# Kernel optimization log

Measured on AMD Instinct MI355X. Metric: run time of the kernel, lower is better.

Reference implementation:

```python
import jax, jax.numpy as jnp
import numpy as np

H = 8
DH = 64
SCALE = DH ** -0.5

def setup_inputs() -> dict:
    key = jax.random.key(0)
    ks = jax.random.split(key, 32)
    B, NQ, N1, N2, N3 = 4, 1024, 1024, 1024, 2048
    QD, C1, C2, C3 = 512, 512, 768, 256
    INNER, VD = H * DH, 512
    s = 0.02
    inp = {
        'x':        jax.random.normal(ks[0], (B, NQ, QD), jnp.float32),
        'context':  jax.random.normal(ks[1], (B, N1, C1), jnp.float32),
        'context2': jax.random.normal(ks[2], (B, N2, C2), jnp.float32),
        'context3': jax.random.normal(ks[3], (B, N3, C3), jnp.float32),
        'mask1': jax.random.randint(ks[4], (B, NQ, N1), 0, 2) > 0,
        'mask2': jax.random.randint(ks[5], (B, NQ, N2), 0, 2) > 0,
        'mask3': jax.random.randint(ks[6], (B, NQ, N3), 0, 2) > 0,
        'Wq':  jax.random.normal(ks[7],  (QD, INNER), jnp.float32) * s,
        'bq':  jnp.zeros((INNER,), jnp.float32),
        'Wk1': jax.random.normal(ks[8],  (C1, INNER), jnp.float32) * s,
        'bk1': jnp.zeros((INNER,), jnp.float32),
        'Wv1': jax.random.normal(ks[9],  (C1, VD), jnp.float32) * s,
        'bv1': jnp.zeros((VD,), jnp.float32),
        'Wk2': jax.random.normal(ks[10], (C2, INNER), jnp.float32) * s,
        'bk2': jnp.zeros((INNER,), jnp.float32),
        'Wv2': jax.random.normal(ks[11], (C2, VD), jnp.float32) * s,
        'bv2': jnp.zeros((VD,), jnp.float32),
        'Wk3': jax.random.normal(ks[12], (C3, INNER), jnp.float32) * s,
        'bk3': jnp.zeros((INNER,), jnp.float32),
        'Wv3': jax.random.normal(ks[13], (C3, VD), jnp.float32) * s,
        'bv3': jnp.zeros((VD,), jnp.float32),
        'Wo':  jax.random.normal(ks[14], (VD, VD), jnp.float32) * s,
        'bo':  jnp.zeros((VD,), jnp.float32),
    }
    return inp

def _split_heads(t):
    # [b, n, h*d] -> [b, h, n, d]
    b, n, hd = t.shape
    return t.reshape(b, n, H, hd // H).transpose(0, 2, 1, 3)

def reference(x, context, context2, context3, mask1, mask2, mask3,
              Wq, bq, Wk1, bk1, Wv1, bv1, Wk2, bk2, Wv2, bv2,
              Wk3, bk3, Wv3, bv3, Wo, bo):
    q = x @ Wq + bq
    k = jnp.concatenate([context @ Wk1 + bk1, context2 @ Wk2 + bk2, context3 @ Wk3 + bk3], axis=1)
    v = jnp.concatenate([context @ Wv1 + bv1, context2 @ Wv2 + bv2, context3 @ Wv3 + bv3], axis=1)
    qh, kh, vh = _split_heads(q), _split_heads(k), _split_heads(v)
    sim = jnp.einsum('bhid,bhjd->bhij', qh, kh) * SCALE  # [b,h,nq,nk]
    mask = jnp.concatenate([mask1, mask2, mask3], axis=2)  # [b,nq,nk]
    neg = -jnp.finfo(sim.dtype).max
    sim = jnp.where(mask[:, None, :, :], sim, neg)
    attn = jax.nn.softmax(sim, axis=-1)
    out = jnp.einsum('bhij,bhjd->bhid', attn, vh)  # [b,h,nq,dv]
    b, h, n, d = out.shape
    out = out.transpose(0, 2, 1, 3).reshape(b, n, h * d)
    return out @ Wo + bo
```

## Files before the change

### kernel.cpp

```cpp
#include <hip/hip_runtime.h>

typedef _Float16 f16;
typedef _Float16 f16x8 __attribute__((ext_vector_type(8)));
typedef _Float16 f16x4 __attribute__((ext_vector_type(4)));
typedef float f32x4 __attribute__((ext_vector_type(4)));
typedef unsigned long long u64;

#define MFMA16(a, b, c) __builtin_amdgcn_mfma_f32_16x16x32_f16((a), (b), (c), 0, 0, 0)

constexpr float QSCALE = 0.18033688011112042f;

struct CDesc { const float* src; f16* dst; unsigned n4, off4; };

__global__ __launch_bounds__(256) void convert_kernel(CDesc a, CDesc b, CDesc c, CDesc d) {
  unsigned t = blockIdx.x * 256u + threadIdx.x;
  CDesc s;
  if (t >= d.off4) s = d;
  else if (t >= c.off4) s = c;
  else if (t >= b.off4) s = b;
  else s = a;
  unsigned i = t - s.off4;
  if (i >= s.n4) return;
  float4 v = ((const float4*)s.src)[i];
  f16x4 o;
  o[0] = (f16)v.x; o[1] = (f16)v.y; o[2] = (f16)v.z; o[3] = (f16)v.w;
  ((f16x4*)s.dst)[i] = o;
}

struct TDesc { const float* src; f16* dst; int K, blk_off; };
struct TArgs { TDesc t[8]; };

__global__ __launch_bounds__(256) void transpose_kernel(TArgs args) {
  int bid = blockIdx.x;
  int di = 0;
#pragma unroll
  for (int i = 1; i < 8; i++)
    if (bid >= args.t[i].blk_off) di = i;
  TDesc d = args.t[di];
  int lb = bid - d.blk_off;
  int ktiles = d.K >> 5;
  int kt = lb % ktiles, nt = lb / ktiles;
  int k0 = kt * 32, n0 = nt * 32;
  __shared__ float tile[32][33];
  int tc = threadIdx.x & 31;
  int tr = threadIdx.x >> 5;
#pragma unroll
  for (int i = 0; i < 4; i++) {
    int kl = tr + 8 * i;
    tile[tc][kl] = d.src[(size_t)(k0 + kl) * 512 + n0 + tc];
  }
  __syncthreads();
#pragma unroll
  for (int i = 0; i < 4; i++) {
    int nl = tr + 8 * i;
    d.dst[(size_t)(n0 + nl) * d.K + k0 + tc] = (f16)tile[nl][tc];
  }
}

__global__ __launch_bounds__(256) void maskprep_kernel(const void* __restrict__ m1,
                                                       const void* __restrict__ m2,
                                                       const void* __restrict__ m3,
                                                       u64* __restrict__ mb) {
  unsigned t = blockIdx.x * 256u + threadIdx.x;
  unsigned probe = ((const unsigned*)m1)[threadIdx.x & 15];
  u64 vote = __ballot(probe <= 1u);
  bool int_mode = ((vote & 0xFFFFull) == 0xFFFFull);
  unsigned row = t >> 12;
  unsigned j = t & 4095;
  const void* src;
  long idx;
  if (j < 1024) { src = m1; idx = (long)row * 1024 + j; }
  else if (j < 2048) { src = m2; idx = (long)row * 1024 + (j - 1024); }
  else { src = m3; idx = (long)row * 2048 + (j - 2048); }
  bool pred = int_mode ? (((const int*)src)[idx] != 0)
                       : (((const unsigned char*)src)[idx] != 0);
  u64 bal = __ballot(pred);
  if ((threadIdx.x & 63) == 0) mb[t >> 6] = bal;
}

struct PDesc {
  const f16* A; const f16* B; const float* bias; void* out;
  int K, mode, logNloc, nk_off, blk_off, ntiles;
};
struct PArgs { PDesc d[8]; };

__global__ __launch_bounds__(256) void proj_kernel(PArgs args, int bid_base) {
  int bid = blockIdx.x + bid_base;
  int di = 0;
#pragma unroll
  for (int i = 1; i < 8; i++)
    if (bid >= args.d[i].blk_off) di = i;
  PDesc d = args.d[di];
  int lb = bid - d.blk_off;
  int bn = lb % d.ntiles, bm = lb / d.ntiles;
  int tid = threadIdx.x;
  int lane = tid & 63, wv = tid >> 6;
  int wm = wv >> 1, wn = wv & 1;
  int r16 = lane & 15, q4 = lane >> 4;
  int K = d.K;
  int m0 = bm * 128, n0 = bn * 128;

  __shared__ f16 As[2][128 * 40];
  __shared__ f16 Bs[2][128 * 40];

  int sr = tid >> 2;
  int sc = (tid & 3) * 8;
  const f16* ag = d.A + (size_t)(m0 + sr) * K + sc;
  const f16* bg = d.B + (size_t)(n0 + sr) * K + sc;
  f16x8 ra0, ra1, rb0, rb1;
  auto ldg = [&](int k0) {
    ra0 = *(const f16x8*)(ag + k0);
    ra1 = *(const f16x8*)(ag + (size_t)64 * K + k0);
    rb0 = *(const f16x8*)(bg + k0);
    rb1 = *(const f16x8*)(bg + (size_t)64 * K + k0);
  };
  auto sts = [&](int p) {
    *(f16x8*)(As[p] + sr * 40 + sc) = ra0;
    *(f16x8*)(As[p] + (sr + 64) * 40 + sc) = ra1;
    *(f16x8*)(Bs[p] + sr * 40 + sc) = rb0;
    *(f16x8*)(Bs[p] + (sr + 64) * 40 + sc) = rb1;
  };

  f32x4 c[4][4] = {};
  int nk = K >> 5;
  ldg(0);
  sts(0);
  __syncthreads();
  for (int kt = 0; kt < nk; kt++) {
    int p = kt & 1;
    if (kt + 1 < nk) ldg((kt + 1) << 5);
    const f16* ab = As[p] + (wm * 64 + r16) * 40 + q4 * 8;
    const f16* bb = Bs[p] + (wn * 64 + r16) * 40 + q4 * 8;
    f16x8 af[4], bf[4];
#pragma unroll
    for (int t = 0; t < 4; t++) af[t] = *(const f16x8*)(ab + t * 16 * 40);
#pragma unroll
    for (int u = 0; u < 4; u++) bf[u] = *(const f16x8*)(bb + u * 16 * 40);
#pragma unroll
    for (int t = 0; t < 4; t++)
#pragma unroll
      for (int u = 0; u < 4; u++) c[t][u] = MFMA16(af[t], bf[u], c[t][u]);
    if (kt + 1 < nk) sts(p ^ 1);
    __syncthreads();
  }

  int msk = (1 << d.logNloc) - 1;
#pragma unroll
  for (int t = 0; t < 4; t++) {
#pragma unroll
    for (int u = 0; u < 4; u++) {
#pragma unroll
      for (int r = 0; r < 4; r++) {
        int gm = m0 + wm * 64 + t * 16 + q4 * 4 + r;
        int cn = n0 + wn * 64 + u * 16 + r16;
        float val = c[t][u][r] + (d.mode == 2 ? d.bias[gm] : d.bias[cn]);
        if (d.mode == 0) {
          int hh = cn >> 6, dd = cn & 63, bb = gm >> 10, nn = gm & 1023;
          ((f16*)d.out)[(((size_t)bb * 8 + hh) * 1024 + nn) * 64 + dd] = (f16)(val * QSCALE);
        } else if (d.mode == 1) {
          int hh = cn >> 6, dd = cn & 63, bb = gm >> d.logNloc, nn = d.nk_off + (gm & msk);
          ((f16*)d.out)[(((size_t)bb * 8 + hh) * 4096 + nn) * 64 + dd] = (f16)val;
        } else if (d.mode == 2) {
          int hh = gm >> 6, dd = gm & 63, bb = cn >> d.logNloc, nn = d.nk_off + (cn & msk);
          ((f16*)d.out)[(((size_t)bb * 8 + hh) * 64 + dd) * 4096 + nn] = (f16)val;
        } else {
          ((float*)d.out)[(size_t)gm * 512 + cn] = val;
        }
      }
    }
  }
}

__global__ __launch_bounds__(256) void attn_kernel(const f16* __restrict__ Qh,
                                                   const f16* __restrict__ Kh,
                                                   const f16* __restrict__ Vt,
                                                   const u64* __restrict__ MB,
                                                   f16* __restrict__ AO) {
  int lin = blockIdx.x;
  int hb = lin & 31, qt = lin >> 5;
  int h = hb & 7, b = hb >> 3;
  int tid = threadIdx.x;
  int lane = tid & 63, wv = tid >> 6;
  int r16 = lane & 15, q4 = lane >> 4;
  int q0 = qt * 64;
  int bh = b * 8 + h;
  const f16* qp = Qh + ((size_t)bh * 1024 + q0 + wv * 16) * 64;
  f16x8 aq0 = *(const f16x8*)(qp + r16 * 64 + q4 * 8);
  f16x8 aq1 = *(const f16x8*)(qp + r16 * 64 + q4 * 8 + 32);
  const f16* kg = Kh + (size_t)bh * (4096 * 64);
  const f16* vg = Vt + (size_t)bh * (64 * 4096);
  const u64* mrow = MB + ((size_t)b * 1024 + q0 + wv * 16 + q4 * 4) * 64;

  __shared__ f16 kls[2][64 * 72];
  __shared__ f16 vls[2][64 * 72];
  __shared__ f16 pbuf[4][16 * 72];
  f16* pw = pbuf[wv];

  int c_row = tid >> 3;
  int c_col = (tid & 7) * 8;
  f16x8 kr0, kr1, vr0, vr1;
  auto loadKV = [&](int j0) {
    const f16* kp = kg + (size_t)(j0 + c_row) * 64 + c_col;
    kr0 = *(const f16x8*)kp;
    kr1 = *(const f16x8*)(kp + 32 * 64);
    const f16* vp = vg + (size_t)c_row * 4096 + j0 + c_col;
    vr0 = *(const f16x8*)vp;
    vr1 = *(const f16x8*)(vp + 32 * 4096);
  };
  auto writeKV = [&](int p) {
    *(f16x8*)(kls[p] + c_row * 72 + c_col) = kr0;
    *(f16x8*)(kls[p] + (c_row + 32) * 72 + c_col) = kr1;
    *(f16x8*)(vls[p] + c_row * 72 + c_col) = vr0;
    *(f16x8*)(vls[p] + (c_row + 32) * 72 + c_col) = vr1;
  };

  f16x8 ones;
#pragma unroll
  for (int i = 0; i < 8; i++) ones[i] = (f16)1.0f;
  f32x4 accl{};
  f32x4 acc[4] = {};

  loadKV(0);
  writeKV(0);
  loadKV(64);
  __syncthreads();

  for (int jt = 0; jt < 64; jt++) {
    int p = jt & 1;
    if (jt < 63) writeKV(p ^ 1);
    if (jt < 62) loadKV((jt + 2) * 64);
    u64 wrd[4];
#pragma unroll
    for (int r = 0; r < 4; r++) wrd[r] = mrow[r * 64 + jt];
    const f16* kb_ = kls[p];
    const f16* vb_ = vls[p];
#pragma unroll
    for (int t = 0; t < 4; t++) {
      f16x8 k0 = *(const f16x8*)(kb_ + (t * 16 + r16) * 72 + q4 * 8);
      f16x8 k1 = *(const f16x8*)(kb_ + (t * 16 + r16) * 72 + q4 * 8 + 32);
      f32x4 z{};
      z = MFMA16(aq0, k0, z);
      z = MFMA16(aq1, k1, z);
#pragma unroll
      for (int r = 0; r < 4; r++) {
        float pv = ((wrd[r] >> (r16 + t * 16)) & 1) ? __builtin_amdgcn_exp2f(z[r]) : 0.0f;
        pw[(q4 * 4 + r) * 72 + t * 16 + r16] = (f16)pv;
      }
    }
    asm volatile("s_waitcnt lgkmcnt(0)" ::: "memory");
    f16x8 ap0 = *(const f16x8*)(pw + r16 * 72 + q4 * 8);
    f16x8 ap1 = *(const f16x8*)(pw + r16 * 72 + q4 * 8 + 32);
#pragma unroll
    for (int dt = 0; dt < 4; dt++) {
      f16x8 v0 = *(const f16x8*)(vb_ + (dt * 16 + r16) * 72 + q4 * 8);
      f16x8 v1 = *(const f16x8*)(vb_ + (dt * 16 + r16) * 72 + q4 * 8 + 32);
      acc[dt] = MFMA16(ap0, v0, acc[dt]);
      acc[dt] = MFMA16(ap1, v1, acc[dt]);
    }
    accl = MFMA16(ap0, ones, accl);
    accl = MFMA16(ap1, ones, accl);
    __syncthreads();
  }

#pragma unroll
  for (int r = 0; r < 4; r++) {
    float inv = 1.0f / accl[r];
    int row = q0 + wv * 16 + q4 * 4 + r;
    f16* orow = AO + ((size_t)b * 1024 + row) * 512 + h * 64 + r16;
#pragma unroll
    for (int dt = 0; dt < 4; dt++) orow[dt * 16] = (f16)(acc[dt][r] * inv);
  }
}

extern "C" void kernel_launch(void* const* d_in, const int* in_sizes, int n_in,
                              void* d_out, int out_size, void* d_ws, size_t ws_size,
                              hipStream_t stream) {
  (void)in_sizes; (void)n_in; (void)out_size; (void)ws_size;
  const float* x  = (const float*)d_in[0];
  const float* c1 = (const float*)d_in[1];
  const float* c2 = (const float*)d_in[2];
  const float* c3 = (const float*)d_in[3];
  const void* m1 = d_in[4];
  const void* m2 = d_in[5];
  const void* m3 = d_in[6];
  const float* Wq = (const float*)d_in[7];   const float* bq = (const float*)d_in[8];
  const float* Wk1 = (const float*)d_in[9];  const float* bk1 = (const float*)d_in[10];
  const float* Wv1 = (const float*)d_in[11]; const float* bv1 = (const float*)d_in[12];
  const float* Wk2 = (const float*)d_in[13]; const float* bk2 = (const float*)d_in[14];
  const float* Wv2 = (const float*)d_in[15]; const float* bv2 = (const float*)d_in[16];
  const float* Wk3 = (const float*)d_in[17]; const float* bk3 = (const float*)d_in[18];
  const float* Wv3 = (const float*)d_in[19]; const float* bv3 = (const float*)d_in[20];
  const float* Wo = (const float*)d_in[21];  const float* bo = (const float*)d_in[22];

  char* ws = (char*)d_ws;
  size_t off = 0;
  auto alloc = [&](size_t bytes) {
    void* p = ws + off;
    off = (off + bytes + 255) & ~(size_t)255;
    return p;
  };
  f16* xb   = (f16*)alloc(2097152 * 2);
  f16* c1b  = (f16*)alloc(2097152 * 2);
  f16* c2b  = (f16*)alloc(3145728 * 2);
  f16* c3b  = (f16*)alloc(2097152 * 2);
  f16* wqt  = (f16*)alloc(262144 * 2);
  f16* wk1t = (f16*)alloc(262144 * 2);
  f16* wk2t = (f16*)alloc(393216 * 2);
  f16* wk3t = (f16*)alloc(131072 * 2);
  f16* wv1t = (f16*)alloc(262144 * 2);
  f16* wv2t = (f16*)alloc(393216 * 2);
  f16* wv3t = (f16*)alloc(131072 * 2);
  f16* wot  = (f16*)alloc(262144 * 2);
  f16* qh   = (f16*)alloc(2097152 * 2);
  f16* kh   = (f16*)alloc(8388608 * 2);
  f16* vt   = (f16*)alloc(8388608 * 2);
  f16* ao   = (f16*)alloc(2097152 * 2);
  u64* mbits = (u64*)alloc(2097152);

  CDesc cdx  = {x,  xb,  524288, 0};
  CDesc cdc1 = {c1, c1b, 524288, 524288};
  CDesc cdc2 = {c2, c2b, 786432, 1048576};
  CDesc cdc3 = {c3, c3b, 524288, 1835008};
  convert_kernel<<<9216, 256, 0, stream>>>(cdx, cdc1, cdc2, cdc3);

  TArgs ta;
  ta.t[0] = {Wq,  wqt,  512, 0};
  ta.t[1] = {Wk1, wk1t, 512, 256};
  ta.t[2] = {Wk2, wk2t, 768, 512};
  ta.t[3] = {Wk3, wk3t, 256, 896};
  ta.t[4] = {Wv1, wv1t, 512, 1024};
  ta.t[5] = {Wv2, wv2t, 768, 1280};
  ta.t[6] = {Wv3, wv3t, 256, 1664};
  ta.t[7] = {Wo,  wot,  512, 1792};
  transpose_kernel<<<2048, 256, 0, stream>>>(ta);

  maskprep_kernel<<<65536, 256, 0, stream>>>(m1, m2, m3, mbits);

  PArgs pa;
  pa.d[0] = {xb,   wqt,  bq,  qh,    512, 0, 10, 0,    0,    4};
  pa.d[1] = {c1b,  wk1t, bk1, kh,    512, 1, 10, 0,    128,  4};
  pa.d[2] = {c2b,  wk2t, bk2, kh,    768, 1, 10, 1024, 256,  4};
  pa.d[3] = {c3b,  wk3t, bk3, kh,    256, 1, 11, 2048, 384,  4};
  pa.d[4] = {wv1t, c1b,  bv1, vt,    512, 2, 10, 0,    640,  32};
  pa.d[5] = {wv2t, c2b,  bv2, vt,    768, 2, 10, 1024, 768,  32};
  pa.d[6] = {wv3t, c3b,  bv3, vt,    256, 2, 11, 2048, 896,  64};
  pa.d[7] = {ao,   wot,  bo,  d_out, 512, 3, 10, 0,    1152, 4};
  proj_kernel<<<1152, 256, 0, stream>>>(pa, 0);

  attn_kernel<<<512, 256, 0, stream>>>(qh, kh, vt, mbits, ao);

  proj_kernel<<<128, 256, 0, stream>>>(pa, 1152);
}
```

Before: 376.4 us.

## Split attention over key chunks with 128-query tiles and a combine kernel

The attention kernel now splits the 4096 keys into four 1024-key chunks handled by separate blocks, doubling the grid so more blocks can run across the CUs. Each block now covers 128 queries, two 16-row subtiles per wave, so every K/V tile staged in shared memory is reused for twice as many queries. P·V now runs in two 32-key halves with a smaller P buffer, and launch bounds request 3 blocks per CU. Unnormalised partial outputs (fp16) and row sums are written to workspace that appears to reuse the converted-input buffers, and a new combine kernel sums the four partials and normalises. In exchange there is an extra kernel launch, extra global traffic for the partials, and a risk of fp16 precision or overflow in the unnormalised sums.

```diff
diff --git a/kernel.cpp b/kernel.cpp
--- a/kernel.cpp
+++ b/kernel.cpp
@@ -171,29 +171,37 @@
   }
 }
 
-__global__ __launch_bounds__(256) void attn_kernel(const f16* __restrict__ Qh,
-                                                   const f16* __restrict__ Kh,
-                                                   const f16* __restrict__ Vt,
-                                                   const u64* __restrict__ MB,
-                                                   f16* __restrict__ AO) {
+__global__ __launch_bounds__(256, 3) void attn_kernel(const f16* __restrict__ Qh,
+                                                      const f16* __restrict__ Kh,
+                                                      const f16* __restrict__ Vt,
+                                                      const u64* __restrict__ MB,
+                                                      f16* __restrict__ PO,
+                                                      float* __restrict__ LW) {
   int lin = blockIdx.x;
-  int hb = lin & 31, qt = lin >> 5;
+  int hb = lin & 31;
+  int rest = lin >> 5;
+  int qt = rest & 7, ks = rest >> 3;
   int h = hb & 7, b = hb >> 3;
   int tid = threadIdx.x;
   int lane = tid & 63, wv = tid >> 6;
   int r16 = lane & 15, q4 = lane >> 4;
-  int q0 = qt * 64;
+  int q0 = qt * 128;
   int bh = b * 8 + h;
-  const f16* qp = Qh + ((size_t)bh * 1024 + q0 + wv * 16) * 64;
-  f16x8 aq0 = *(const f16x8*)(qp + r16 * 64 + q4 * 8);
-  f16x8 aq1 = *(const f16x8*)(qp + r16 * 64 + q4 * 8 + 32);
-  const f16* kg = Kh + (size_t)bh * (4096 * 64);
-  const f16* vg = Vt + (size_t)bh * (64 * 4096);
-  const u64* mrow = MB + ((size_t)b * 1024 + q0 + wv * 16 + q4 * 4) * 64;
+
+  const f16* qp = Qh + ((size_t)bh * 1024 + q0 + wv * 32) * 64;
+  f16x8 aq[2][2];
+#pragma unroll
+  for (int s = 0; s < 2; s++) {
+    aq[s][0] = *(const f16x8*)(qp + (s * 16 + r16) * 64 + q4 * 8);
+    aq[s][1] = *(const f16x8*)(qp + (s * 16 + r16) * 64 + q4 * 8 + 32);
+  }
+  const f16* kg = Kh + (size_t)bh * (4096 * 64) + (size_t)ks * 1024 * 64;
+  const f16* vg = Vt + (size_t)bh * (64 * 4096) + ks * 1024;
+  const u64* mrow = MB + ((size_t)b * 1024 + q0 + wv * 32 + q4 * 4) * 64 + ks * 16;
 
   __shared__ f16 kls[2][64 * 72];
   __shared__ f16 vls[2][64 * 72];
-  __shared__ f16 pbuf[4][16 * 72];
+  __shared__ f16 pbuf[4][32 * 40];
   f16* pw = pbuf[wv];
 
   int c_row = tid >> 3;
@@ -217,59 +225,102 @@
   f16x8 ones;
 #pragma unroll
   for (int i = 0; i < 8; i++) ones[i] = (f16)1.0f;
-  f32x4 accl{};
-  f32x4 acc[4] = {};
+  f32x4 accl[2] = {};
+  f32x4 acc[2][4] = {};
 
   loadKV(0);
   writeKV(0);
   loadKV(64);
   __syncthreads();
 
-  for (int jt = 0; jt < 64; jt++) {
+  for (int jt = 0; jt < 16; jt++) {
     int p = jt & 1;
-    if (jt < 63) writeKV(p ^ 1);
-    if (jt < 62) loadKV((jt + 2) * 64);
-    u64 wrd[4];
-#pragma unroll
-    for (int r = 0; r < 4; r++) wrd[r] = mrow[r * 64 + jt];
+    if (jt < 15) writeKV(p ^ 1);
+    if (jt < 14) loadKV((jt + 2) * 64);
+    u64 wrd[2][4];
+#pragma unroll
+    for (int s = 0; s < 2; s++)
+#pragma unroll
+      for (int r = 0; r < 4; r++) wrd[s][r] = mrow[(s * 16 + r) * 64 + jt];
     const f16* kb_ = kls[p];
     const f16* vb_ = vls[p];
 #pragma unroll
-    for (int t = 0; t < 4; t++) {
-      f16x8 k0 = *(const f16x8*)(kb_ + (t * 16 + r16) * 72 + q4 * 8);
-      f16x8 k1 = *(const f16x8*)(kb_ + (t * 16 + r16) * 72 + q4 * 8 + 32);
-      f32x4 z{};
-      z = MFMA16(aq0, k0, z);
-      z = MFMA16(aq1, k1, z);
-#pragma unroll
-      for (int r = 0; r < 4; r++) {
-        float pv = ((wrd[r] >> (r16 + t * 16)) & 1) ? __builtin_amdgcn_exp2f(z[r]) : 0.0f;
-        pw[(q4 * 4 + r) * 72 + t * 16 + r16] = (f16)pv;
+    for (int ph = 0; ph < 2; ph++) {
+#pragma unroll
+      for (int th = 0; th < 2; th++) {
+        int t = ph * 2 + th;
+        f16x8 k0 = *(const f16x8*)(kb_ + (t * 16 + r16) * 72 + q4 * 8);
+        f16x8 k1 = *(const f16x8*)(kb_ + (t * 16 + r16) * 72 + q4 * 8 + 32);
+#pragma unroll
+        for (int s = 0; s < 2; s++) {
+          f32x4 z{};
+          z = MFMA16(aq[s][0], k0, z);
+          z = MFMA16(aq[s][1], k1, z);
+#pragma unroll
+          for (int r = 0; r < 4; r++) {
+            float pv = ((wrd[s][r] >> (r16 + t * 16)) & 1)
+                           ? __builtin_amdgcn_exp2f(z[r]) : 0.0f;
+            pw[(s * 16 + q4 * 4 + r) * 40 + th * 16 + r16] = (f16)pv;
+          }
+        }
       }
+      asm volatile("s_waitcnt lgkmcnt(0)" ::: "memory");
+      f16x8 ap[2];
+#pragma unroll
+      for (int s = 0; s < 2; s++)
+        ap[s] = *(const f16x8*)(pw + (s * 16 + r16) * 40 + q4 * 8);
+#pragma unroll
+      for (int dt = 0; dt < 4; dt++) {
+        f16x8 vf = *(const f16x8*)(vb_ + (dt * 16 + r16) * 72 + ph * 32 + q4 * 8);
+#pragma unroll
+        for (int s = 0; s < 2; s++) acc[s][dt] = MFMA16(ap[s], vf, acc[s][dt]);
+      }
+#pragma unroll
+      for (int s = 0; s < 2; s++) accl[s] = MFMA16(ap[s], ones, accl[s]);
     }
-    asm volatile("s_waitcnt lgkmcnt(0)" ::: "memory");
-    f16x8 ap0 = *(const f16x8*)(pw + r16 * 72 + q4 * 8);
-    f16x8 ap1 = *(const f16x8*)(pw + r16 * 72 + q4 * 8 + 32);
-#pragma unroll
-    for (int dt = 0; dt < 4; dt++) {
-      f16x8 v0 = *(const f16x8*)(vb_ + (dt * 16 + r16) * 72 + q4 * 8);
-      f16x8 v1 = *(const f16x8*)(vb_ + (dt * 16 + r16) * 72 + q4 * 8 + 32);
-      acc[dt] = MFMA16(ap0, v0, acc[dt]);
-      acc[dt] = MFMA16(ap1, v1, acc[dt]);
+    __syncthreads();
+  }
+
+  f16* pok = PO + (size_t)ks * (4096 * 512);
+#pragma unroll
+  for (int s = 0; s < 2; s++)
+#pragma unroll
+    for (int r = 0; r < 4; r++) {
+      int rowg = b * 1024 + q0 + wv * 32 + s * 16 + q4 * 4 + r;
+      f16* orow = pok + (size_t)rowg * 512 + h * 64 + r16;
+#pragma unroll
+      for (int dt = 0; dt < 4; dt++) orow[dt * 16] = (f16)(acc[s][dt][r]);
     }
-    accl = MFMA16(ap0, ones, accl);
-    accl = MFMA16(ap1, ones, accl);
-    __syncthreads();
-  }
-
-#pragma unroll
-  for (int r = 0; r < 4; r++) {
-    float inv = 1.0f / accl[r];
-    int row = q0 + wv * 16 + q4 * 4 + r;
-    f16* orow = AO + ((size_t)b * 1024 + row) * 512 + h * 64 + r16;
-#pragma unroll
-    for (int dt = 0; dt < 4; dt++) orow[dt * 16] = (f16)(acc[dt][r] * inv);
-  }
+  if (r16 == 0) {
+    float* lk = LW + (size_t)ks * 32768 + (size_t)bh * 1024 + q0 + wv * 32;
+#pragma unroll
+    for (int s = 0; s < 2; s++)
+#pragma unroll
+      for (int r = 0; r < 4; r++) lk[s * 16 + q4 * 4 + r] = accl[s][r];
+  }
+}
+
+__global__ __launch_bounds__(256) void combine_kernel(const f16* __restrict__ PO,
+                                                      const float* __restrict__ LW,
+                                                      f16* __restrict__ AO) {
+  int t = blockIdx.x * 256 + threadIdx.x;
+  int row = t >> 6;
+  int col = (t & 63) * 8;
+  int b = row >> 10, q = row & 1023;
+  int h = col >> 6;
+  size_t lidx = (size_t)(b * 8 + h) * 1024 + q;
+  float l = LW[lidx] + LW[32768 + lidx] + LW[65536 + lidx] + LW[98304 + lidx];
+  float inv = 1.0f / l;
+  size_t off = (size_t)row * 512 + col;
+  f16x8 o0 = *(const f16x8*)(PO + off);
+  f16x8 o1 = *(const f16x8*)(PO + 2097152 + off);
+  f16x8 o2 = *(const f16x8*)(PO + 4194304 + off);
+  f16x8 o3 = *(const f16x8*)(PO + 6291456 + off);
+  f16x8 out;
+#pragma unroll
+  for (int j = 0; j < 8; j++)
+    out[j] = (f16)(((float)o0[j] + (float)o1[j] + (float)o2[j] + (float)o3[j]) * inv);
+  *(f16x8*)(AO + off) = out;
 }
 
 extern "C" void kernel_launch(void* const* d_in, const int* in_sizes, int n_in,
@@ -317,6 +368,9 @@
   f16* ao   = (f16*)alloc(2097152 * 2);
   u64* mbits = (u64*)alloc(2097152);
 
+  f16* po = (f16*)ws;
+  float* lw = (float*)(ws + 16777216);
+
   CDesc cdx  = {x,  xb,  524288, 0};
   CDesc cdc1 = {c1, c1b, 524288, 524288};
   CDesc cdc2 = {c2, c2b, 786432, 1048576};
@@ -347,7 +401,9 @@
   pa.d[7] = {ao,   wot,  bo,  d_out, 512, 3, 10, 0,    1152, 4};
   proj_kernel<<<1152, 256, 0, stream>>>(pa, 0);
 
-  attn_kernel<<<512, 256, 0, stream>>>(qh, kh, vt, mbits, ao);
+  attn_kernel<<<1024, 256, 0, stream>>>(qh, kh, vt, mbits, po, lw);
+
+  combine_kernel<<<1024, 256, 0, stream>>>(po, lw, ao);
 
   proj_kernel<<<128, 256, 0, stream>>>(pa, 1152);
 }
```

Result: faster. 360.4 us (-4.3%).
